# Performance work log

Measured on AMD Instinct MI355X. Metric: run time of the kernel, lower is better.

Reference implementation:

```python
import jax, jax.numpy as jnp
import numpy as np

B, H, W, C, N, P = 4, 200, 176, 256, 16384, 65536
EPS = 1e-3  # BatchNorm eps from the torch module


def _bn(x, g, b, axes):
    # training-mode batch norm (batch statistics), matching nn.BatchNorm forward
    m = x.mean(axes, keepdims=True)
    v = x.var(axes, keepdims=True)
    return (x - m) * jax.lax.rsqrt(v + EPS) * g + b


def setup_inputs() -> dict:
    key = jax.random.key(0)
    ks = jax.random.split(key, 16)
    s = 0.05
    d = {}
    d['feats'] = jax.random.normal(ks[0], (B, C, N), jnp.float32)
    d['cb'] = jax.random.randint(ks[1], (P,), 0, B, dtype=jnp.int32)
    d['cy'] = jax.random.randint(ks[2], (P,), 0, H, dtype=jnp.int32)
    d['cx'] = jax.random.randint(ks[3], (P,), 0, W, dtype=jnp.int32)
    # SH head: Linear(256,256,nb)+BN+ReLU, Linear(256,256,nb)+BN+ReLU, Linear(256,9,b)
    d['sh_w1'] = jax.random.normal(ks[4], (C, 256), jnp.float32) * s
    d['sh_g1'] = jnp.ones((256,), jnp.float32); d['sh_b1'] = jnp.zeros((256,), jnp.float32)
    d['sh_w2'] = jax.random.normal(ks[5], (256, 256), jnp.float32) * s
    d['sh_g2'] = jnp.ones((256,), jnp.float32); d['sh_b2'] = jnp.zeros((256,), jnp.float32)
    d['sh_w3'] = jax.random.normal(ks[6], (256, 9), jnp.float32) * s
    d['sh_bias3'] = jnp.zeros((9,), jnp.float32)
    # Gaus head: Linear(256,256,nb)+BN+ReLU, Linear(256,128,nb)+BN+ReLU, Linear(128,1,b)+sigmoid
    d['g_w1'] = jax.random.normal(ks[7], (C, 256), jnp.float32) * s
    d['g_g1'] = jnp.ones((256,), jnp.float32); d['g_b1'] = jnp.zeros((256,), jnp.float32)
    d['g_w2'] = jax.random.normal(ks[8], (256, 128), jnp.float32) * s
    d['g_g2'] = jnp.ones((128,), jnp.float32); d['g_b2'] = jnp.zeros((128,), jnp.float32)
    d['g_w3'] = jax.random.normal(ks[9], (128, 1), jnp.float32) * s
    d['g_bias3'] = jnp.zeros((1,), jnp.float32)
    # conv_out: 3x3 SparseConv2d no-bias + BN + ReLU ; shared_conv: 3x3 SubMConv2d bias + BN + ReLU
    d['cw1'] = jax.random.normal(ks[10], (3, 3, C, C), jnp.float32) * s
    d['c1_g'] = jnp.ones((C,), jnp.float32); d['c1_b'] = jnp.zeros((C,), jnp.float32)
    d['cw2'] = jax.random.normal(ks[11], (3, 3, C, C), jnp.float32) * s
    d['c2_bias'] = jnp.zeros((C,), jnp.float32)
    d['c2_g'] = jnp.ones((C,), jnp.float32); d['c2_b'] = jnp.zeros((C,), jnp.float32)
    return d


def reference(feats, cb, cy, cx, sh_w1, sh_g1, sh_b1, sh_w2, sh_g2, sh_b2, sh_w3, sh_bias3,
              g_w1, g_g1, g_b1, g_w2, g_g2, g_b2, g_w3, g_bias3,
              cw1, c1_g, c1_b, cw2, c2_bias, c2_g, c2_b):
    # [B,C,N] -> [B*N, C] point-wise features
    pw = feats.transpose(0, 2, 1).reshape(-1, C)
    # pool_feature_in_same_voxel: mean of point features sharing a voxel
    vid = cb * (H * W) + cy * W + cx  # [P] linear voxel id over dense BEV grid
    S = B * H * W
    sums = jax.ops.segment_sum(pw, vid, num_segments=S)            # [S, C]
    cnt = jax.ops.segment_sum(jnp.ones((P,), pw.dtype), vid, num_segments=S)
    pooled = sums / jnp.maximum(cnt, 1.0)[:, None]                 # [S, C]
    # SH head
    h = jax.nn.relu(_bn(pooled @ sh_w1, sh_g1, sh_b1, 0))
    h = jax.nn.relu(_bn(h @ sh_w2, sh_g2, sh_b2, 0))
    pred_sh = h @ sh_w3 + sh_bias3                                 # [S, 9]
    # Gaussian head
    g = jax.nn.relu(_bn(pooled @ g_w1, g_g1, g_b1, 0))
    g = jax.nn.relu(_bn(g @ g_w2, g_g2, g_b2, 0))
    pred_gaus = jax.nn.sigmoid(g @ g_w3 + g_bias3)                 # [S, 1]
    # get_sparse_voxel_feature3: SH (DC term) + gaussian modulated voxel features
    sp = pooled * pred_gaus * pred_sh[:, :1]                       # [S, C]
    x = sp.reshape(B, H, W, C)                                      # dense BEV sparse-tensor equivalent
    dn = ('NHWC', 'HWIO', 'NHWC')
    x = jax.lax.conv_general_dilated(x, cw1, (1, 1), 'SAME', dimension_numbers=dn)
    x = jax.nn.relu(_bn(x, c1_g, c1_b, (0, 1, 2)))
    x = jax.lax.conv_general_dilated(x, cw2, (1, 1), 'SAME', dimension_numbers=dn) + c2_bias
    x = jax.nn.relu(_bn(x, c2_g, c2_b, (0, 1, 2)))
    return x
```

## Files before the change

### kernel.cpp

```cpp
#include <hip/hip_runtime.h>
#include <hip/hip_bf16.h>
#include <cstdint>
#include <cstddef>

#define B_DIM 4
#define H_DIM 200
#define W_DIM 176
#define CCH 256
#define NPP 16384
#define NPTS 65536
#define HW 35200
#define S_TOT 140800
#define EPS 1e-3f
#define INV_S (1.0f/140800.0f)

typedef unsigned short ushort_t;
typedef __attribute__((ext_vector_type(8))) short bf16x8;
typedef __attribute__((ext_vector_type(4))) float f32x4;

__device__ __forceinline__ ushort_t f2bf(float f) {
    __hip_bfloat16 h = __float2bfloat16(f);
    return *(ushort_t*)&h;
}
__device__ __forceinline__ float bf2f(ushort_t u) {
    __hip_bfloat16 h = *(__hip_bfloat16*)&u;
    return __bfloat162float(h);
}

__device__ __forceinline__ void async16(const void* g, void* l) {
    __builtin_amdgcn_global_load_lds(
        (const __attribute__((address_space(1))) unsigned int*)g,
        (__attribute__((address_space(3))) unsigned int*)l,
        16, 0, 0);
}

__device__ __forceinline__ void wait_vmcnt0()  { asm volatile("s_waitcnt vmcnt(0)" ::: "memory"); }
__device__ __forceinline__ void wait_vmcnt4()  { asm volatile("s_waitcnt vmcnt(4)" ::: "memory"); }
__device__ __forceinline__ void wait_vmcnt8()  { asm volatile("s_waitcnt vmcnt(8)" ::: "memory"); }
__device__ __forceinline__ void wait_vmcnt10() { asm volatile("s_waitcnt vmcnt(10)" ::: "memory"); }
__device__ __forceinline__ void memfence_compiler() { asm volatile("" ::: "memory"); }

__device__ __forceinline__ int xcd_virt(int fid, int n) {
    int q = n >> 3, r = n & 7;
    int xcd = fid & 7, idx = fid >> 3;
    int base = (xcd < r) ? xcd * (q + 1) : r * (q + 1) + (xcd - r) * q;
    return base + idx;
}

__global__ __launch_bounds__(256) void k_transpose(
    const float* __restrict__ feats, ushort_t* __restrict__ FT)
{
    __shared__ float lds[64][65];
    const int b  = blockIdx.z;
    const int c0 = blockIdx.y * 64;
    const int n0 = blockIdx.x * 64;
    const int tid = threadIdx.x;
#pragma unroll
    for (int i = 0; i < 16; ++i) {
        int idx = i * 256 + tid;
        int cr = idx >> 6, nc = idx & 63;
        lds[cr][nc] = feats[((size_t)b * 256 + c0 + cr) * NPP + n0 + nc];
    }
    __syncthreads();
#pragma unroll
    for (int i = 0; i < 16; ++i) {
        int idx = i * 256 + tid;
        int nr = idx >> 6, cc = idx & 63;
        FT[((size_t)b * NPP + n0 + nr) * CCH + c0 + cc] = f2bf(lds[cc][nr]);
    }
}

__global__ __launch_bounds__(256) void k_buildidx(
    const int* __restrict__ cb, const int* __restrict__ cy,
    const int* __restrict__ cx, int* __restrict__ cnt,
    int* __restrict__ pslot, int* __restrict__ vid)
{
    int p = blockIdx.x * 256 + threadIdx.x;
    int v = cb[p] * HW + cy[p] * W_DIM + cx[p];
    vid[p] = v;
    int r = atomicAdd(&cnt[v], 1);
    if (r < 8) pslot[v * 8 + r] = p;
}

__global__ __launch_bounds__(256) void k_poolgather(
    const ushort_t* __restrict__ FT, const int* __restrict__ cnt,
    const int* __restrict__ pslot, const int* __restrict__ vid,
    ushort_t* __restrict__ Pb)
{
    const int wave = threadIdx.x >> 6;
    const int lane = threadIdx.x & 63;
    const int v = blockIdx.x * 4 + wave;
    const int c = cnt[v];
    float a0 = 0.f, a1 = 0.f, a2 = 0.f, a3 = 0.f;
    if (c <= 8) {
        for (int k = 0; k < c; ++k) {
            int p = pslot[v * 8 + k];
            ushort4 r = ((const ushort4*)(FT + (size_t)p * CCH))[lane];
            a0 += bf2f(r.x); a1 += bf2f(r.y); a2 += bf2f(r.z); a3 += bf2f(r.w);
        }
    } else {
        for (int p = 0; p < NPTS; ++p)
            if (vid[p] == v) {
                ushort4 r = ((const ushort4*)(FT + (size_t)p * CCH))[lane];
                a0 += bf2f(r.x); a1 += bf2f(r.y); a2 += bf2f(r.z); a3 += bf2f(r.w);
            }
    }
    float inv = c ? 1.f / (float)c : 0.f;
    ushort4 o;
    o.x = f2bf(a0 * inv); o.y = f2bf(a1 * inv);
    o.z = f2bf(a2 * inv); o.w = f2bf(a3 * inv);
    ((ushort4*)(Pb + (size_t)v * CCH))[lane] = o;
}

__global__ __launch_bounds__(256) void k_gemmma(
    const ushort_t* __restrict__ X, const ushort_t* __restrict__ Wt,
    ushort_t* __restrict__ Y1, ushort_t* __restrict__ Y2, int ldY,
    int bnh, int nblocks,
    float* __restrict__ acc0, float* __restrict__ acc1, int sqoff)
{
    __shared__ ushort_t Asm[2][128 * 64];
    __shared__ ushort_t Bsm[2][128 * 64];
    const int tid  = threadIdx.x;
    const int w    = tid >> 6;
    const int lane = tid & 63;
    const int virt = xcd_virt(blockIdx.x, nblocks);
    const int pi   = virt / bnh;
    const int bn   = (virt % bnh) * 128;
    const int bm   = pi * 128;
    const int wr   = (w >> 1) * 64;
    const int wc   = (w & 1) * 64;

    size_t aoff[4]; size_t boff[4];
#pragma unroll
    for (int j = 0; j < 4; ++j) {
        int row  = 32 * j + 8 * w + (lane >> 3);
        int qlog = (lane & 7) ^ (row & 7);
        aoff[j] = (size_t)(bm + row) * 256 + qlog * 8;
        boff[j] = (size_t)(bn + row) * 256 + qlog * 8;
    }
    const int lo = (w * 8) * 64;

#pragma unroll
    for (int j = 0; j < 4; ++j) async16(X + aoff[j], &Asm[0][(j * 32) * 64 + lo]);
#pragma unroll
    for (int j = 0; j < 4; ++j) async16(Wt + boff[j], &Bsm[0][(j * 32) * 64 + lo]);

    f32x4 acc[4][4] = {};
    for (int kc = 0; kc < 4; ++kc) {
        if (kc < 3) {
#pragma unroll
            for (int j = 0; j < 4; ++j)
                async16(X + aoff[j] + (kc + 1) * 64, &Asm[(kc + 1) & 1][(j * 32) * 64 + lo]);
#pragma unroll
            for (int j = 0; j < 4; ++j)
                async16(Wt + boff[j] + (kc + 1) * 64, &Bsm[(kc + 1) & 1][(j * 32) * 64 + lo]);
            wait_vmcnt8();
        } else {
            wait_vmcnt0();
        }
        __builtin_amdgcn_s_barrier();
        const ushort_t* Ac = Asm[kc & 1];
        const ushort_t* Bc = Bsm[kc & 1];
        __builtin_amdgcn_s_setprio(1);
#pragma unroll
        for (int ks = 0; ks < 2; ++ks) {
            const int q = ks * 4 + (lane >> 4);
            bf16x8 af[4], bfr[4];
#pragma unroll
            for (int i = 0; i < 4; ++i) {
                int ra = wr + i * 16 + (lane & 15);
                af[i] = *(const bf16x8*)&Ac[ra * 64 + ((q ^ (ra & 7)) * 8)];
            }
#pragma unroll
            for (int jn = 0; jn < 4; ++jn) {
                int rn = wc + jn * 16 + (lane & 15);
                bfr[jn] = *(const bf16x8*)&Bc[rn * 64 + ((q ^ (rn & 7)) * 8)];
            }
#pragma unroll
            for (int i = 0; i < 4; ++i)
#pragma unroll
                for (int jn = 0; jn < 4; ++jn)
                    acc[i][jn] = __builtin_amdgcn_mfma_f32_16x16x32_bf16(
                        af[i], bfr[jn], acc[i][jn], 0, 0, 0);
        }
        __builtin_amdgcn_s_setprio(0);
        memfence_compiler();
        __builtin_amdgcn_s_barrier();
    }
    __syncthreads();

    const int crow0 = bm + wr + (lane >> 4) * 4;
    const int ccol0 = bn + wc + (lane & 15);
    float ls[4] = {}, lq[4] = {};
#pragma unroll
    for (int i = 0; i < 4; ++i)
#pragma unroll
        for (int jn = 0; jn < 4; ++jn) {
            int col = ccol0 + jn * 16;
#pragma unroll
            for (int r = 0; r < 4; ++r) {
                float v = acc[i][jn][r];
                ls[jn] += v; lq[jn] += v * v;
                size_t row = (size_t)(crow0 + i * 16 + r);
                if (col < 256) Y1[row * ldY + col] = f2bf(v);
                else           Y2[row * ldY + col - 256] = f2bf(v);
            }
        }
#pragma unroll
    for (int jn = 0; jn < 4; ++jn) {
        ls[jn] += __shfl_xor(ls[jn], 16, 64); ls[jn] += __shfl_xor(ls[jn], 32, 64);
        lq[jn] += __shfl_xor(lq[jn], 16, 64); lq[jn] += __shfl_xor(lq[jn], 32, 64);
    }
    float* red = (float*)&Asm[0][0];
    if (lane < 16) {
#pragma unroll
        for (int jn = 0; jn < 4; ++jn) {
            red[((w * 16 + lane) * 4 + jn) * 2 + 0] = ls[jn];
            red[((w * 16 + lane) * 4 + jn) * 2 + 1] = lq[jn];
        }
    }
    __syncthreads();
    if (tid < 256) {
        int colhalf = tid & 127, isq = tid >> 7;
        int pair = colhalf >> 6, within = colhalf & 63;
        int l16 = within & 15, jn = within >> 4;
        int w0 = pair ? 1 : 0, w1 = pair ? 3 : 2;
        float s = red[((w0 * 16 + l16) * 4 + jn) * 2 + isq]
                + red[((w1 * 16 + l16) * 4 + jn) * 2 + isq];
        int colg = bn + colhalf;
        float* t = (colg < 256) ? acc0 : acc1;
        atomicAdd(&t[(colg & 255) + isq * sqoff], s);
    }
}

__global__ __launch_bounds__(256) void k_convmma(
    const ushort_t* __restrict__ X, const ushort_t* __restrict__ Wt,
    ushort_t* __restrict__ Yb, const float* __restrict__ bias,
    const ushort_t* __restrict__ zp, float* __restrict__ accp)
{
    __shared__ ushort_t Asm[2][192 * 64];
    __shared__ ushort_t Bsm[2][128 * 64];
    const int tid  = threadIdx.x;
    const int w    = tid >> 6;
    const int lane = tid & 63;
    const int virt = xcd_virt(blockIdx.x, 2200);
    const int pi   = virt >> 1;
    const int bn   = (virt & 1) * 128;
    const int b    = pi / 275;
    const int rem  = pi % 275;
    const int th   = rem / 11, tw = rem % 11;
    const int y0   = th * 8 - 1, x0 = tw * 16 - 1;
    const int hb   = (w >> 1) * 4;
    const int wc   = (w & 1) * 64;

    const int qlog = (lane & 7) ^ (lane >> 3);
    const ushort_t* asrc[6];
#pragma unroll
    for (int j = 0; j < 6; ++j) {
        int hr = j * 32 + w * 8 + (lane >> 3);
        int ph = hr / 18, pw = hr % 18;
        int y = y0 + ph, x = x0 + pw;
        bool ok = (hr < 180) && ((unsigned)y < (unsigned)H_DIM) &&
                  ((unsigned)x < (unsigned)W_DIM);
        asrc[j] = ok ? X + ((size_t)b * HW + (size_t)y * W_DIM + x) * 256 + qlog * 8
                     : zp + (lane & 7) * 8;
    }
    const ushort_t* bsrc = Wt + (size_t)(bn + w * 8 + (lane >> 3)) * 256 + qlog * 8;
    const int lo = (w * 8) * 64;

#pragma unroll
    for (int j = 0; j < 6; ++j)
        async16(asrc[j], &Asm[0][(j * 32) * 64 + lo]);
#pragma unroll
    for (int j = 0; j < 4; ++j)
        async16(bsrc + (size_t)j * 8192, &Bsm[0][(j * 32) * 64 + lo]);

    f32x4 acc[4][4] = {};
    for (int kc = 0; kc < 4; ++kc) {
        const ushort_t* acur = Asm[kc & 1];
#pragma unroll
        for (int pos = 0; pos < 9; ++pos) {
            const ushort_t* bcur = Bsm[(kc + pos) & 1];
            ushort_t* bnxt = (ushort_t*)Bsm[(kc + pos + 1) & 1];
            if (pos == 0) {
                if (kc < 3) {
#pragma unroll
                    for (int j = 0; j < 6; ++j)
                        async16(asrc[j] + (kc + 1) * 64,
                                &Asm[(kc + 1) & 1][(j * 32) * 64 + lo]);
#pragma unroll
                    for (int j = 0; j < 4; ++j)
                        async16(bsrc + (size_t)65536 + kc * 64 + j * 8192,
                                bnxt + (j * 32) * 64 + lo);
                    wait_vmcnt10();
                } else {
#pragma unroll
                    for (int j = 0; j < 4; ++j)
                        async16(bsrc + (size_t)65536 + kc * 64 + j * 8192,
                                bnxt + (j * 32) * 64 + lo);
                    wait_vmcnt4();
                }
            } else if (pos < 8) {
#pragma unroll
                for (int j = 0; j < 4; ++j)
                    async16(bsrc + (size_t)(pos + 1) * 65536 + kc * 64 + j * 8192,
                            bnxt + (j * 32) * 64 + lo);
                wait_vmcnt4();
            } else if (kc < 3) {
#pragma unroll
                for (int j = 0; j < 4; ++j)
                    async16(bsrc + (size_t)(kc + 1) * 64 + j * 8192,
                            bnxt + (j * 32) * 64 + lo);
                wait_vmcnt4();
            } else {
                wait_vmcnt0();
            }
            __builtin_amdgcn_s_barrier();
            const int dy = pos / 3 - 1, dx = pos % 3 - 1;
            __builtin_amdgcn_s_setprio(1);
#pragma unroll
            for (int ks = 0; ks < 2; ++ks) {
                const int q = ks * 4 + (lane >> 4);
                bf16x8 af[4], bfr[4];
#pragma unroll
                for (int i = 0; i < 4; ++i) {
                    int ri = (hb + i + 1 + dy) * 18 + 1 + dx + (lane & 15);
                    af[i] = *(const bf16x8*)&acur[ri * 64 + ((q ^ (ri & 7)) * 8)];
                }
#pragma unroll
                for (int jn = 0; jn < 4; ++jn) {
                    int rn = wc + jn * 16 + (lane & 15);
                    bfr[jn] = *(const bf16x8*)&bcur[rn * 64 + ((q ^ (rn & 7)) * 8)];
                }
#pragma unroll
                for (int i = 0; i < 4; ++i)
#pragma unroll
                    for (int jn = 0; jn < 4; ++jn)
                        acc[i][jn] = __builtin_amdgcn_mfma_f32_16x16x32_bf16(
                            af[i], bfr[jn], acc[i][jn], 0, 0, 0);
            }
            __builtin_amdgcn_s_setprio(0);
            memfence_compiler();
            __builtin_amdgcn_s_barrier();
        }
    }
    __syncthreads();

    const size_t sbase = (size_t)b * HW + (size_t)(th * 8) * W_DIM + tw * 16;
    const int colb = bn + wc + (lane & 15);
    const int wsub = (lane >> 4) * 4;
    float ls[4] = {}, lq[4] = {};
#pragma unroll
    for (int i = 0; i < 4; ++i) {
        int h = hb + i;
#pragma unroll
        for (int jn = 0; jn < 4; ++jn) {
            int col = colb + jn * 16;
            float bb = bias ? bias[col] : 0.f;
#pragma unroll
            for (int r = 0; r < 4; ++r) {
                size_t s = sbase + (size_t)h * W_DIM + wsub + r;
                float v = acc[i][jn][r] + bb;
                ls[jn] += v; lq[jn] += v * v;
                Yb[s * 256 + col] = f2bf(v);
            }
        }
    }
#pragma unroll
    for (int jn = 0; jn < 4; ++jn) {
        ls[jn] += __shfl_xor(ls[jn], 16, 64); ls[jn] += __shfl_xor(ls[jn], 32, 64);
        lq[jn] += __shfl_xor(lq[jn], 16, 64); lq[jn] += __shfl_xor(lq[jn], 32, 64);
    }
    float* red = (float*)&Asm[0][0];
    if (lane < 16) {
#pragma unroll
        for (int jn = 0; jn < 4; ++jn) {
            red[((w * 16 + lane) * 4 + jn) * 2 + 0] = ls[jn];
            red[((w * 16 + lane) * 4 + jn) * 2 + 1] = lq[jn];
        }
    }
    __syncthreads();
    if (tid < 256) {
        int colhalf = tid & 127, isq = tid >> 7;
        int pair = colhalf >> 6, within = colhalf & 63;
        int l16 = within & 15, jn = within >> 4;
        int w0 = pair ? 1 : 0, w1 = pair ? 3 : 2;
        float s = red[((w0 * 16 + l16) * 4 + jn) * 2 + isq]
                + red[((w1 * 16 + l16) * 4 + jn) * 2 + isq];
        atomicAdd(&accp[(bn + colhalf) + isq * 256], s);
    }
}

__global__ __launch_bounds__(256) void k_castw(
    const float* __restrict__ Wc, ushort_t* __restrict__ Wt, int CO)
{
    int pc = blockIdx.x;
    int co = pc % CO, pos = pc / CO, ci = threadIdx.x;
    Wt[(size_t)pc * 256 + ci] = f2bf(Wc[((size_t)pos * 256 + ci) * CO + co]);
}

__global__ void k_bnparams(const float* __restrict__ acc,
                           const float* __restrict__ g,
                           const float* __restrict__ b,
                           float* __restrict__ par, int ncols)
{
    int c = threadIdx.x;
    if (c >= ncols) return;
    float m = acc[c] * INV_S;
    float v = acc[ncols + c] * INV_S - m * m;
    float sc = g[c] * rsqrtf(v + EPS);
    par[c] = sc;
    par[ncols + c] = b[c] - m * sc;
}

__global__ __launch_bounds__(256) void k_bnrelu_bf(
    ushort_t* __restrict__ Y, const float* __restrict__ par)
{
    size_t q = (size_t)blockIdx.x * 256 + threadIdx.x;
    int c = (int)(q & 63) * 4;
    ushort4 u = ((ushort4*)Y)[q];
    u.x = f2bf(fmaxf(0.f, bf2f(u.x) * par[c + 0] + par[256 + c + 0]));
    u.y = f2bf(fmaxf(0.f, bf2f(u.y) * par[c + 1] + par[256 + c + 1]));
    u.z = f2bf(fmaxf(0.f, bf2f(u.z) * par[c + 2] + par[256 + c + 2]));
    u.w = f2bf(fmaxf(0.f, bf2f(u.w) * par[c + 3] + par[256 + c + 3]));
    ((ushort4*)Y)[q] = u;
}

__global__ __launch_bounds__(256) void k_headfin(
    const ushort_t* __restrict__ B2, const ushort_t* __restrict__ B3,
    const float* __restrict__ par1, const float* __restrict__ par3,
    const float* __restrict__ shw3, const float* __restrict__ shb3,
    const float* __restrict__ gw3, const float* __restrict__ gb3,
    const ushort_t* __restrict__ Pb, ushort_t* __restrict__ Xb)
{
    const int wave = threadIdx.x >> 6;
    const int lane = threadIdx.x & 63;
    const int s = blockIdx.x * 4 + wave;
    const ushort_t* b2 = B2 + (size_t)s * 256;
    const ushort_t* b3 = B3 + (size_t)s * 128;
    float d1 = 0.f, d2 = 0.f;
    {
        ushort4 u = ((const ushort4*)b2)[lane];
        int c = lane * 4;
        float v0 = fmaxf(0.f, bf2f(u.x) * par1[c + 0] + par1[256 + c + 0]);
        float v1 = fmaxf(0.f, bf2f(u.y) * par1[c + 1] + par1[256 + c + 1]);
        float v2 = fmaxf(0.f, bf2f(u.z) * par1[c + 2] + par1[256 + c + 2]);
        float v3 = fmaxf(0.f, bf2f(u.w) * par1[c + 3] + par1[256 + c + 3]);
        d1 = v0 * shw3[(c + 0) * 9] + v1 * shw3[(c + 1) * 9]
           + v2 * shw3[(c + 2) * 9] + v3 * shw3[(c + 3) * 9];
    }
    {
        ushort2 u = ((const ushort2*)b3)[lane];
        int c = lane * 2;
        float v0 = fmaxf(0.f, bf2f(u.x) * par3[c + 0] + par3[128 + c + 0]);
        float v1 = fmaxf(0.f, bf2f(u.y) * par3[c + 1] + par3[128 + c + 1]);
        d2 = v0 * gw3[c + 0] + v1 * gw3[c + 1];
    }
#pragma unroll
    for (int off = 32; off > 0; off >>= 1) {
        d1 += __shfl_down(d1, off, 64);
        d2 += __shfl_down(d2, off, 64);
    }
    d1 = __shfl(d1, 0, 64);
    d2 = __shfl(d2, 0, 64);
    float shdc = d1 + shb3[0];
    float gaus = 1.f / (1.f + expf(-(d2 + gb3[0])));
    float factor = shdc * gaus;
    ushort4 pv = ((const ushort4*)(Pb + (size_t)s * 256))[lane];
    ushort4 o;
    o.x = f2bf(bf2f(pv.x) * factor);
    o.y = f2bf(bf2f(pv.y) * factor);
    o.z = f2bf(bf2f(pv.z) * factor);
    o.w = f2bf(bf2f(pv.w) * factor);
    ((ushort4*)(Xb + (size_t)s * 256))[lane] = o;
}

__global__ __launch_bounds__(256) void k_bnrelu_f32out(
    const ushort_t* __restrict__ Y, const float* __restrict__ par,
    float* __restrict__ out)
{
    size_t q = (size_t)blockIdx.x * 256 + threadIdx.x;
    int c = (int)(q & 63) * 4;
    ushort4 u = ((const ushort4*)Y)[q];
    float4 v;
    v.x = fmaxf(0.f, bf2f(u.x) * par[c + 0] + par[256 + c + 0]);
    v.y = fmaxf(0.f, bf2f(u.y) * par[c + 1] + par[256 + c + 1]);
    v.z = fmaxf(0.f, bf2f(u.z) * par[c + 2] + par[256 + c + 2]);
    v.w = fmaxf(0.f, bf2f(u.w) * par[c + 3] + par[256 + c + 3]);
    ((float4*)out)[q] = v;
}

extern "C" void kernel_launch(void* const* d_in, const int* in_sizes, int n_in,
                              void* d_out, int out_size, void* d_ws, size_t ws_size,
                              hipStream_t stream)
{
    (void)in_sizes; (void)n_in; (void)out_size; (void)ws_size;
    const float* feats   = (const float*)d_in[0];
    const int*   cb      = (const int*)d_in[1];
    const int*   cy      = (const int*)d_in[2];
    const int*   cx      = (const int*)d_in[3];
    const float* sh_w1   = (const float*)d_in[4];
    const float* sh_g1   = (const float*)d_in[5];
    const float* sh_b1   = (const float*)d_in[6];
    const float* sh_w2   = (const float*)d_in[7];
    const float* sh_g2   = (const float*)d_in[8];
    const float* sh_b2   = (const float*)d_in[9];
    const float* sh_w3   = (const float*)d_in[10];
    const float* sh_bias3= (const float*)d_in[11];
    const float* g_w1    = (const float*)d_in[12];
    const float* g_g1    = (const float*)d_in[13];
    const float* g_b1    = (const float*)d_in[14];
    const float* g_w2    = (const float*)d_in[15];
    const float* g_g2    = (const float*)d_in[16];
    const float* g_b2    = (const float*)d_in[17];
    const float* g_w3    = (const float*)d_in[18];
    const float* g_bias3 = (const float*)d_in[19];
    const float* cw1     = (const float*)d_in[20];
    const float* c1_g    = (const float*)d_in[21];
    const float* c1_b    = (const float*)d_in[22];
    const float* cw2     = (const float*)d_in[23];
    const float* c2_bias = (const float*)d_in[24];
    const float* c2_g    = (const float*)d_in[25];
    const float* c2_b    = (const float*)d_in[26];

    float* out = (float*)d_out;
    float* ws  = (float*)d_ws;
    ushort_t* Pb   = (ushort_t*)(ws);
    ushort_t* Bsh  = (ushort_t*)(ws + 18022400);
    ushort_t* Bg   = (ushort_t*)(ws + 36044800);
    ushort_t* Cb   = (ushort_t*)(ws + 54067200);
    ushort_t* FT   = (ushort_t*)(ws + 54067200);
    ushort_t* Db   = (ushort_t*)(ws + 72089600);
    int*      CNTi = (int*)(ws + 72089600);
    int*      PSL  = CNTi + S_TOT;
    int*      VID  = PSL + S_TOT * 8;
    ushort_t* Eb   = Pb;
    ushort_t* WCAT = (ushort_t*)(ws + 81100800);
    ushort_t* WS2  = WCAT + 131072;
    ushort_t* WG2  = WS2 + 65536;
    ushort_t* WT1  = WG2 + 32768;
    ushort_t* WT2  = WT1 + 589824;
    ushort_t* ZP   = WT2 + 589824;
    float*    ACC  = (float*)(ZP + 2048);
    float*    PAR  = ACC + 6 * 512;

    hipMemsetAsync(CNTi, 0, (size_t)S_TOT * 4, stream);
    hipMemsetAsync(ACC, 0, 6 * 512 * 4, stream);
    hipMemsetAsync(ZP, 0, 4096, stream);

    k_castw<<<256, 256, 0, stream>>>(sh_w1, WCAT, 256);
    k_castw<<<256, 256, 0, stream>>>(g_w1, WCAT + 65536, 256);
    k_castw<<<256, 256, 0, stream>>>(sh_w2, WS2, 256);
    k_castw<<<128, 256, 0, stream>>>(g_w2, WG2, 128);
    k_castw<<<9 * 256, 256, 0, stream>>>(cw1, WT1, 256);
    k_castw<<<9 * 256, 256, 0, stream>>>(cw2, WT2, 256);

    k_transpose<<<dim3(256, 4, 4), 256, 0, stream>>>(feats, FT);
    k_buildidx<<<NPTS / 256, 256, 0, stream>>>(cb, cy, cx, CNTi, PSL, VID);
    k_poolgather<<<S_TOT / 4, 256, 0, stream>>>(FT, CNTi, PSL, VID, Pb);

    k_gemmma<<<4400, 256, 0, stream>>>(Pb, WCAT, Bsh, Bg, 256, 4, 4400,
                                       ACC + 0 * 512, ACC + 2 * 512, 256);
    k_bnparams<<<1, 256, 0, stream>>>(ACC + 0 * 512, sh_g1, sh_b1, PAR + 0 * 512, 256);
    k_bnparams<<<1, 256, 0, stream>>>(ACC + 2 * 512, g_g1, g_b1, PAR + 2 * 512, 256);
    k_bnrelu_bf<<<35200, 256, 0, stream>>>(Bsh, PAR + 0 * 512);
    k_bnrelu_bf<<<35200, 256, 0, stream>>>(Bg, PAR + 2 * 512);
    k_gemmma<<<2200, 256, 0, stream>>>(Bsh, WS2, Cb, Cb, 256, 2, 2200,
                                       ACC + 1 * 512, ACC + 1 * 512, 256);
    k_bnparams<<<1, 256, 0, stream>>>(ACC + 1 * 512, sh_g2, sh_b2, PAR + 1 * 512, 256);
    k_gemmma<<<1100, 256, 0, stream>>>(Bg, WG2, Db, Db, 128, 1, 1100,
                                       ACC + 3 * 512, ACC + 3 * 512, 128);
    k_bnparams<<<1, 128, 0, stream>>>(ACC + 3 * 512, g_g2, g_b2, PAR + 3 * 512, 128);
    k_headfin<<<S_TOT / 4, 256, 0, stream>>>(Cb, Db, PAR + 1 * 512, PAR + 3 * 512,
                                             sh_w3, sh_bias3, g_w3, g_bias3, Pb, Bsh);
    k_convmma<<<2200, 256, 0, stream>>>(Bsh, WT1, Eb, nullptr, ZP, ACC + 4 * 512);
    k_bnparams<<<1, 256, 0, stream>>>(ACC + 4 * 512, c1_g, c1_b, PAR + 4 * 512, 256);
    k_bnrelu_bf<<<35200, 256, 0, stream>>>(Eb, PAR + 4 * 512);
    k_convmma<<<2200, 256, 0, stream>>>(Eb, WT2, Bsh, c2_bias, ZP, ACC + 5 * 512);
    k_bnparams<<<1, 256, 0, stream>>>(ACC + 5 * 512, c2_g, c2_b, PAR + 5 * 512, 256);
    k_bnrelu_f32out<<<35200, 256, 0, stream>>>(Bsh, PAR + 5 * 512, out);
}
```

Baseline: 811.6 us.

## Fuse BatchNorm+ReLU into consumer GEMM/conv loads and fold BN param kernels

```diff
diff --git a/kernel.cpp b/kernel.cpp
--- a/kernel.cpp
+++ b/kernel.cpp
@@ -38,7 +38,19 @@
 __device__ __forceinline__ void wait_vmcnt4()  { asm volatile("s_waitcnt vmcnt(4)" ::: "memory"); }
 __device__ __forceinline__ void wait_vmcnt8()  { asm volatile("s_waitcnt vmcnt(8)" ::: "memory"); }
 __device__ __forceinline__ void wait_vmcnt10() { asm volatile("s_waitcnt vmcnt(10)" ::: "memory"); }
+__device__ __forceinline__ void wait_lgkm0()   { asm volatile("s_waitcnt lgkmcnt(0)" ::: "memory"); }
 __device__ __forceinline__ void memfence_compiler() { asm volatile("" ::: "memory"); }
+
+__device__ __forceinline__ bf16x8 bnrelu8(bf16x8 a, const float* __restrict__ sc,
+                                          const float* __restrict__ sh) {
+    bf16x8 r;
+#pragma unroll
+    for (int e = 0; e < 8; ++e) {
+        float f = bf2f((ushort_t)a[e]);
+        r[e] = (short)f2bf(fmaxf(0.f, f * sc[e] + sh[e]));
+    }
+    return r;
+}
 
 __device__ __forceinline__ int xcd_virt(int fid, int n) {
     int q = n >> 3, r = n & 7;
@@ -230,6 +242,154 @@
         int colg = bn + colhalf;
         float* t = (colg < 256) ? acc0 : acc1;
         atomicAdd(&t[(colg & 255) + isq * sqoff], s);
+    }
+}
+
+__global__ __launch_bounds__(256) void k_gemmma_bn(
+    const ushort_t* __restrict__ X, const float* __restrict__ accIn,
+    const float* __restrict__ gIn, const float* __restrict__ bIn,
+    const ushort_t* __restrict__ Wt,
+    ushort_t* __restrict__ Y, int ldY, int bnh, int nblocks,
+    float* __restrict__ accOut, int sqoff)
+{
+    __shared__ ushort_t Asm[2][128 * 64];
+    __shared__ ushort_t Bsm[2][128 * 64];
+    __shared__ float parS[512];
+    const int tid  = threadIdx.x;
+    const int w    = tid >> 6;
+    const int lane = tid & 63;
+    {
+        float m = accIn[tid] * INV_S;
+        float v = accIn[256 + tid] * INV_S - m * m;
+        float sc = gIn[tid] * rsqrtf(v + EPS);
+        parS[tid] = sc;
+        parS[256 + tid] = bIn[tid] - m * sc;
+    }
+    __syncthreads();
+
+    const int virt = xcd_virt(blockIdx.x, nblocks);
+    const int pi   = virt / bnh;
+    const int bn   = (virt % bnh) * 128;
+    const int bm   = pi * 128;
+    const int wr   = (w >> 1) * 64;
+    const int wc   = (w & 1) * 64;
+
+    const int qlog = (lane & 7) ^ ((8 * w + (lane >> 3)) & 7);
+    size_t aoff[4]; size_t boff[4]; int arow[4];
+#pragma unroll
+    for (int j = 0; j < 4; ++j) {
+        int row  = 32 * j + 8 * w + (lane >> 3);
+        arow[j] = row;
+        aoff[j] = (size_t)(bm + row) * 256 + qlog * 8;
+        boff[j] = (size_t)(bn + row) * 256 + qlog * 8;
+    }
+    const int lo = (w * 8) * 64;
+    const int lsub = (lane & 7) * 8;
+
+    bf16x8 ar[2][4];
+#pragma unroll
+    for (int j = 0; j < 4; ++j) async16(Wt + boff[j], &Bsm[0][(j * 32) * 64 + lo]);
+#pragma unroll
+    for (int j = 0; j < 4; ++j) ar[0][j] = *(const bf16x8*)(X + aoff[j]);
+    {
+        const int cb = qlog * 8;
+#pragma unroll
+        for (int j = 0; j < 4; ++j)
+            *(bf16x8*)&Asm[0][arow[j] * 64 + lsub] =
+                bnrelu8(ar[0][j], parS + cb, parS + 256 + cb);
+    }
+    wait_lgkm0();
+
+    f32x4 acc[4][4] = {};
+#pragma unroll
+    for (int kc = 0; kc < 4; ++kc) {
+        if (kc < 3) {
+#pragma unroll
+            for (int j = 0; j < 4; ++j)
+                async16(Wt + boff[j] + (kc + 1) * 64, &Bsm[(kc + 1) & 1][(j * 32) * 64 + lo]);
+#pragma unroll
+            for (int j = 0; j < 4; ++j)
+                ar[(kc + 1) & 1][j] = *(const bf16x8*)(X + aoff[j] + (kc + 1) * 64);
+            wait_vmcnt8();
+        } else {
+            wait_vmcnt0();
+        }
+        __builtin_amdgcn_s_barrier();
+        const ushort_t* Ac = Asm[kc & 1];
+        const ushort_t* Bc = Bsm[kc & 1];
+        __builtin_amdgcn_s_setprio(1);
+#pragma unroll
+        for (int ks = 0; ks < 2; ++ks) {
+            const int q = ks * 4 + (lane >> 4);
+            bf16x8 af[4], bfr[4];
+#pragma unroll
+            for (int i = 0; i < 4; ++i) {
+                int ra = wr + i * 16 + (lane & 15);
+                af[i] = *(const bf16x8*)&Ac[ra * 64 + ((q ^ (ra & 7)) * 8)];
+            }
+#pragma unroll
+            for (int jn = 0; jn < 4; ++jn) {
+                int rn = wc + jn * 16 + (lane & 15);
+                bfr[jn] = *(const bf16x8*)&Bc[rn * 64 + ((q ^ (rn & 7)) * 8)];
+            }
+#pragma unroll
+            for (int i = 0; i < 4; ++i)
+#pragma unroll
+                for (int jn = 0; jn < 4; ++jn)
+                    acc[i][jn] = __builtin_amdgcn_mfma_f32_16x16x32_bf16(
+                        af[i], bfr[jn], acc[i][jn], 0, 0, 0);
+        }
+        __builtin_amdgcn_s_setprio(0);
+        if (kc < 3) {
+            const int cb = (kc + 1) * 64 + qlog * 8;
+#pragma unroll
+            for (int j = 0; j < 4; ++j)
+                *(bf16x8*)&Asm[(kc + 1) & 1][arow[j] * 64 + lsub] =
+                    bnrelu8(ar[(kc + 1) & 1][j], parS + cb, parS + 256 + cb);
+            wait_lgkm0();
+        }
+        memfence_compiler();
+        __builtin_amdgcn_s_barrier();
+    }
+    __syncthreads();
+
+    const int crow0 = bm + wr + (lane >> 4) * 4;
+    const int ccol0 = bn + wc + (lane & 15);
+    float ls[4] = {}, lq[4] = {};
+#pragma unroll
+    for (int i = 0; i < 4; ++i)
+#pragma unroll
+        for (int jn = 0; jn < 4; ++jn) {
+            int col = ccol0 + jn * 16;
+#pragma unroll
+            for (int r = 0; r < 4; ++r) {
+                float v = acc[i][jn][r];
+                ls[jn] += v; lq[jn] += v * v;
+                Y[(size_t)(crow0 + i * 16 + r) * ldY + col] = f2bf(v);
+            }
+        }
+#pragma unroll
+    for (int jn = 0; jn < 4; ++jn) {
+        ls[jn] += __shfl_xor(ls[jn], 16, 64); ls[jn] += __shfl_xor(ls[jn], 32, 64);
+        lq[jn] += __shfl_xor(lq[jn], 16, 64); lq[jn] += __shfl_xor(lq[jn], 32, 64);
+    }
+    float* red = (float*)&Asm[0][0];
+    if (lane < 16) {
+#pragma unroll
+        for (int jn = 0; jn < 4; ++jn) {
+            red[((w * 16 + lane) * 4 + jn) * 2 + 0] = ls[jn];
+            red[((w * 16 + lane) * 4 + jn) * 2 + 1] = lq[jn];
+        }
+    }
+    __syncthreads();
+    if (tid < 256) {
+        int colhalf = tid & 127, isq = tid >> 7;
+        int pair = colhalf >> 6, within = colhalf & 63;
+        int l16 = within & 15, jn = within >> 4;
+        int w0 = pair ? 1 : 0, w1 = pair ? 3 : 2;
+        float s = red[((w0 * 16 + l16) * 4 + jn) * 2 + isq]
+                + red[((w1 * 16 + l16) * 4 + jn) * 2 + isq];
+        atomicAdd(&accOut[(bn + colhalf) + isq * sqoff], s);
     }
 }
 
@@ -391,6 +551,173 @@
     }
 }
 
+__global__ __launch_bounds__(256) void k_convmma_bn(
+    const ushort_t* __restrict__ X, const float* __restrict__ par,
+    const ushort_t* __restrict__ Wt,
+    ushort_t* __restrict__ Yb, const float* __restrict__ bias,
+    const ushort_t* __restrict__ zp, float* __restrict__ accp)
+{
+    __shared__ ushort_t Asm[2][192 * 64];
+    __shared__ ushort_t Bsm[2][128 * 64];
+    const int tid  = threadIdx.x;
+    const int w    = tid >> 6;
+    const int lane = tid & 63;
+    const int virt = xcd_virt(blockIdx.x, 2200);
+    const int pi   = virt >> 1;
+    const int bn   = (virt & 1) * 128;
+    const int b    = pi / 275;
+    const int rem  = pi % 275;
+    const int th   = rem / 11, tw = rem % 11;
+    const int y0   = th * 8 - 1, x0 = tw * 16 - 1;
+    const int hb   = (w >> 1) * 4;
+    const int wc   = (w & 1) * 64;
+
+    const int qlog = (lane & 7) ^ (lane >> 3);
+    const ushort_t* asrc[6];
+    bool okj[6];
+    int arow[6];
+#pragma unroll
+    for (int j = 0; j < 6; ++j) {
+        int hr = j * 32 + w * 8 + (lane >> 3);
+        arow[j] = hr;
+        int ph = hr / 18, pw = hr % 18;
+        int y = y0 + ph, x = x0 + pw;
+        okj[j] = (hr < 180) && ((unsigned)y < (unsigned)H_DIM) &&
+                 ((unsigned)x < (unsigned)W_DIM);
+        asrc[j] = okj[j] ? X + ((size_t)b * HW + (size_t)y * W_DIM + x) * 256 + qlog * 8
+                         : zp + (lane & 7) * 8;
+    }
+    const ushort_t* bsrc = Wt + (size_t)(bn + w * 8 + (lane >> 3)) * 256 + qlog * 8;
+    const int lo = (w * 8) * 64;
+    const int lsub = (lane & 7) * 8;
+    const bf16x8 zv = 0;
+
+    bf16x8 areg[6];
+#pragma unroll
+    for (int j = 0; j < 6; ++j) areg[j] = *(const bf16x8*)(asrc[j]);
+#pragma unroll
+    for (int j = 0; j < 4; ++j)
+        async16(bsrc + (size_t)j * 8192, &Bsm[0][(j * 32) * 64 + lo]);
+    {
+        const int cb = qlog * 8;
+#pragma unroll
+        for (int j = 0; j < 6; ++j)
+            *(bf16x8*)&Asm[0][arow[j] * 64 + lsub] =
+                okj[j] ? bnrelu8(areg[j], par + cb, par + 256 + cb) : zv;
+    }
+    wait_lgkm0();
+
+    f32x4 acc[4][4] = {};
+#pragma unroll
+    for (int kc = 0; kc < 4; ++kc) {
+        const ushort_t* acur = Asm[kc & 1];
+#pragma unroll
+        for (int pos = 0; pos < 9; ++pos) {
+            const ushort_t* bcur = Bsm[(kc + pos) & 1];
+            ushort_t* bnxt = (ushort_t*)Bsm[(kc + pos + 1) & 1];
+            if (pos < 8) {
+#pragma unroll
+                for (int j = 0; j < 4; ++j)
+                    async16(bsrc + (size_t)(pos + 1) * 65536 + kc * 64 + j * 8192,
+                            bnxt + (j * 32) * 64 + lo);
+            } else if (kc < 3) {
+#pragma unroll
+                for (int j = 0; j < 4; ++j)
+                    async16(bsrc + (size_t)(kc + 1) * 64 + j * 8192,
+                            bnxt + (j * 32) * 64 + lo);
+            }
+            if (pos == 5 && kc < 3) {
+#pragma unroll
+                for (int j = 0; j < 6; ++j)
+                    areg[j] = *(const bf16x8*)(asrc[j] + (kc + 1) * 64);
+            }
+            if (kc == 3 && pos == 8)      wait_vmcnt0();
+            else if (pos == 6 && kc < 3)  wait_vmcnt10();
+            else                          wait_vmcnt4();
+            __builtin_amdgcn_s_barrier();
+            const int dy = pos / 3 - 1, dx = pos % 3 - 1;
+            __builtin_amdgcn_s_setprio(1);
+#pragma unroll
+            for (int ks = 0; ks < 2; ++ks) {
+                const int q = ks * 4 + (lane >> 4);
+                bf16x8 af[4], bfr[4];
+#pragma unroll
+                for (int i = 0; i < 4; ++i) {
+                    int ri = (hb + i + 1 + dy) * 18 + 1 + dx + (lane & 15);
+                    af[i] = *(const bf16x8*)&acur[ri * 64 + ((q ^ (ri & 7)) * 8)];
+                }
+#pragma unroll
+                for (int jn = 0; jn < 4; ++jn) {
+                    int rn = wc + jn * 16 + (lane & 15);
+                    bfr[jn] = *(const bf16x8*)&bcur[rn * 64 + ((q ^ (rn & 7)) * 8)];
+                }
+#pragma unroll
+                for (int i = 0; i < 4; ++i)
+#pragma unroll
+                    for (int jn = 0; jn < 4; ++jn)
+                        acc[i][jn] = __builtin_amdgcn_mfma_f32_16x16x32_bf16(
+                            af[i], bfr[jn], acc[i][jn], 0, 0, 0);
+            }
+            __builtin_amdgcn_s_setprio(0);
+            if (pos == 8 && kc < 3) {
+                const int cb = (kc + 1) * 64 + qlog * 8;
+#pragma unroll
+                for (int j = 0; j < 6; ++j)
+                    *(bf16x8*)&Asm[(kc + 1) & 1][arow[j] * 64 + lsub] =
+                        okj[j] ? bnrelu8(areg[j], par + cb, par + 256 + cb) : zv;
+                wait_lgkm0();
+            }
+            memfence_compiler();
+            __builtin_amdgcn_s_barrier();
+        }
+    }
+    __syncthreads();
+
+    const size_t sbase = (size_t)b * HW + (size_t)(th * 8) * W_DIM + tw * 16;
+    const int colb = bn + wc + (lane & 15);
+    const int wsub = (lane >> 4) * 4;
+    float ls[4] = {}, lq[4] = {};
+#pragma unroll
+    for (int i = 0; i < 4; ++i) {
+        int h = hb + i;
+#pragma unroll
+        for (int jn = 0; jn < 4; ++jn) {
+            int col = colb + jn * 16;
+            float bb = bias ? bias[col] : 0.f;
+#pragma unroll
+            for (int r = 0; r < 4; ++r) {
+                size_t s = sbase + (size_t)h * W_DIM + wsub + r;
+                float v = acc[i][jn][r] + bb;
+                ls[jn] += v; lq[jn] += v * v;
+                Yb[s * 256 + col] = f2bf(v);
+            }
+        }
+    }
+#pragma unroll
+    for (int jn = 0; jn < 4; ++jn) {
+        ls[jn] += __shfl_xor(ls[jn], 16, 64); ls[jn] += __shfl_xor(ls[jn], 32, 64);
+        lq[jn] += __shfl_xor(lq[jn], 16, 64); lq[jn] += __shfl_xor(lq[jn], 32, 64);
+    }
+    float* red = (float*)&Asm[0][0];
+    if (lane < 16) {
+#pragma unroll
+        for (int jn = 0; jn < 4; ++jn) {
+            red[((w * 16 + lane) * 4 + jn) * 2 + 0] = ls[jn];
+            red[((w * 16 + lane) * 4 + jn) * 2 + 1] = lq[jn];
+        }
+    }
+    __syncthreads();
+    if (tid < 256) {
+        int colhalf = tid & 127, isq = tid >> 7;
+        int pair = colhalf >> 6, within = colhalf & 63;
+        int l16 = within & 15, jn = within >> 4;
+        int w0 = pair ? 1 : 0, w1 = pair ? 3 : 2;
+        float s = red[((w0 * 16 + l16) * 4 + jn) * 2 + isq]
+                + red[((w1 * 16 + l16) * 4 + jn) * 2 + isq];
+        atomicAdd(&accp[(bn + colhalf) + isq * 256], s);
+    }
+}
+
 __global__ __launch_bounds__(256) void k_castw(
     const float* __restrict__ Wc, ushort_t* __restrict__ Wt, int CO)
 {
@@ -413,28 +740,34 @@
     par[ncols + c] = b[c] - m * sc;
 }
 
-__global__ __launch_bounds__(256) void k_bnrelu_bf(
-    ushort_t* __restrict__ Y, const float* __restrict__ par)
-{
-    size_t q = (size_t)blockIdx.x * 256 + threadIdx.x;
-    int c = (int)(q & 63) * 4;
-    ushort4 u = ((ushort4*)Y)[q];
-    u.x = f2bf(fmaxf(0.f, bf2f(u.x) * par[c + 0] + par[256 + c + 0]));
-    u.y = f2bf(fmaxf(0.f, bf2f(u.y) * par[c + 1] + par[256 + c + 1]));
-    u.z = f2bf(fmaxf(0.f, bf2f(u.z) * par[c + 2] + par[256 + c + 2]));
-    u.w = f2bf(fmaxf(0.f, bf2f(u.w) * par[c + 3] + par[256 + c + 3]));
-    ((ushort4*)Y)[q] = u;
-}
-
 __global__ __launch_bounds__(256) void k_headfin(
     const ushort_t* __restrict__ B2, const ushort_t* __restrict__ B3,
-    const float* __restrict__ par1, const float* __restrict__ par3,
+    const float* __restrict__ acc1, const float* __restrict__ shg2,
+    const float* __restrict__ shb2,
+    const float* __restrict__ acc3, const float* __restrict__ gg2,
+    const float* __restrict__ gb2,
     const float* __restrict__ shw3, const float* __restrict__ shb3,
     const float* __restrict__ gw3, const float* __restrict__ gb3,
     const ushort_t* __restrict__ Pb, ushort_t* __restrict__ Xb)
 {
-    const int wave = threadIdx.x >> 6;
-    const int lane = threadIdx.x & 63;
+    __shared__ float parA[512], parB[256];
+    const int t = threadIdx.x;
+    {
+        float m = acc1[t] * INV_S;
+        float v = acc1[256 + t] * INV_S - m * m;
+        float sc = shg2[t] * rsqrtf(v + EPS);
+        parA[t] = sc; parA[256 + t] = shb2[t] - m * sc;
+    }
+    if (t < 128) {
+        float m = acc3[t] * INV_S;
+        float v = acc3[128 + t] * INV_S - m * m;
+        float sc = gg2[t] * rsqrtf(v + EPS);
+        parB[t] = sc; parB[128 + t] = gb2[t] - m * sc;
+    }
+    __syncthreads();
+
+    const int wave = t >> 6;
+    const int lane = t & 63;
     const int s = blockIdx.x * 4 + wave;
     const ushort_t* b2 = B2 + (size_t)s * 256;
     const ushort_t* b3 = B3 + (size_t)s * 128;
@@ -442,18 +775,18 @@
     {
         ushort4 u = ((const ushort4*)b2)[lane];
         int c = lane * 4;
-        float v0 = fmaxf(0.f, bf2f(u.x) * par1[c + 0] + par1[256 + c + 0]);
-        float v1 = fmaxf(0.f, bf2f(u.y) * par1[c + 1] + par1[256 + c + 1]);
-        float v2 = fmaxf(0.f, bf2f(u.z) * par1[c + 2] + par1[256 + c + 2]);
-        float v3 = fmaxf(0.f, bf2f(u.w) * par1[c + 3] + par1[256 + c + 3]);
+        float v0 = fmaxf(0.f, bf2f(u.x) * parA[c + 0] + parA[256 + c + 0]);
+        float v1 = fmaxf(0.f, bf2f(u.y) * parA[c + 1] + parA[256 + c + 1]);
+        float v2 = fmaxf(0.f, bf2f(u.z) * parA[c + 2] + parA[256 + c + 2]);
+        float v3 = fmaxf(0.f, bf2f(u.w) * parA[c + 3] + parA[256 + c + 3]);
         d1 = v0 * shw3[(c + 0) * 9] + v1 * shw3[(c + 1) * 9]
            + v2 * shw3[(c + 2) * 9] + v3 * shw3[(c + 3) * 9];
     }
     {
         ushort2 u = ((const ushort2*)b3)[lane];
         int c = lane * 2;
-        float v0 = fmaxf(0.f, bf2f(u.x) * par3[c + 0] + par3[128 + c + 0]);
-        float v1 = fmaxf(0.f, bf2f(u.y) * par3[c + 1] + par3[128 + c + 1]);
+        float v0 = fmaxf(0.f, bf2f(u.x) * parB[c + 0] + parB[128 + c + 0]);
+        float v1 = fmaxf(0.f, bf2f(u.y) * parB[c + 1] + parB[128 + c + 1]);
         d2 = v0 * gw3[c + 0] + v1 * gw3[c + 1];
     }
 #pragma unroll
@@ -476,10 +809,20 @@
 }
 
 __global__ __launch_bounds__(256) void k_bnrelu_f32out(
-    const ushort_t* __restrict__ Y, const float* __restrict__ par,
+    const ushort_t* __restrict__ Y, const float* __restrict__ acc5,
+    const float* __restrict__ g, const float* __restrict__ b,
     float* __restrict__ out)
 {
-    size_t q = (size_t)blockIdx.x * 256 + threadIdx.x;
+    __shared__ float par[512];
+    const int t = threadIdx.x;
+    {
+        float m = acc5[t] * INV_S;
+        float v = acc5[256 + t] * INV_S - m * m;
+        float sc = g[t] * rsqrtf(v + EPS);
+        par[t] = sc; par[256 + t] = b[t] - m * sc;
+    }
+    __syncthreads();
+    size_t q = (size_t)blockIdx.x * 256 + t;
     int c = (int)(q & 63) * 4;
     ushort4 u = ((const ushort4*)Y)[q];
     float4 v;
@@ -561,22 +904,20 @@
 
     k_gemmma<<<4400, 256, 0, stream>>>(Pb, WCAT, Bsh, Bg, 256, 4, 4400,
                                        ACC + 0 * 512, ACC + 2 * 512, 256);
-    k_bnparams<<<1, 256, 0, stream>>>(ACC + 0 * 512, sh_g1, sh_b1, PAR + 0 * 512, 256);
-    k_bnparams<<<1, 256, 0, stream>>>(ACC + 2 * 512, g_g1, g_b1, PAR + 2 * 512, 256);
-    k_bnrelu_bf<<<35200, 256, 0, stream>>>(Bsh, PAR + 0 * 512);
-    k_bnrelu_bf<<<35200, 256, 0, stream>>>(Bg, PAR + 2 * 512);
-    k_gemmma<<<2200, 256, 0, stream>>>(Bsh, WS2, Cb, Cb, 256, 2, 2200,
-                                       ACC + 1 * 512, ACC + 1 * 512, 256);
-    k_bnparams<<<1, 256, 0, stream>>>(ACC + 1 * 512, sh_g2, sh_b2, PAR + 1 * 512, 256);
-    k_gemmma<<<1100, 256, 0, stream>>>(Bg, WG2, Db, Db, 128, 1, 1100,
-                                       ACC + 3 * 512, ACC + 3 * 512, 128);
-    k_bnparams<<<1, 128, 0, stream>>>(ACC + 3 * 512, g_g2, g_b2, PAR + 3 * 512, 128);
-    k_headfin<<<S_TOT / 4, 256, 0, stream>>>(Cb, Db, PAR + 1 * 512, PAR + 3 * 512,
-                                             sh_w3, sh_bias3, g_w3, g_bias3, Pb, Bsh);
+    k_gemmma_bn<<<2200, 256, 0, stream>>>(Bsh, ACC + 0 * 512, sh_g1, sh_b1,
+                                          WS2, Cb, 256, 2, 2200,
+                                          ACC + 1 * 512, 256);
+    k_gemmma_bn<<<1100, 256, 0, stream>>>(Bg, ACC + 2 * 512, g_g1, g_b1,
+                                          WG2, Db, 128, 1, 1100,
+                                          ACC + 3 * 512, 128);
+    k_headfin<<<S_TOT / 4, 256, 0, stream>>>(Cb, Db,
+                                             ACC + 1 * 512, sh_g2, sh_b2,
+                                             ACC + 3 * 512, g_g2, g_b2,
+                                             sh_w3, sh_bias3, g_w3, g_bias3,
+                                             Pb, Bsh);
     k_convmma<<<2200, 256, 0, stream>>>(Bsh, WT1, Eb, nullptr, ZP, ACC + 4 * 512);
-    k_bnparams<<<1, 256, 0, stream>>>(ACC + 4 * 512, c1_g, c1_b, PAR + 4 * 512, 256);
-    k_bnrelu_bf<<<35200, 256, 0, stream>>>(Eb, PAR + 4 * 512);
-    k_convmma<<<2200, 256, 0, stream>>>(Eb, WT2, Bsh, c2_bias, ZP, ACC + 5 * 512);
-    k_bnparams<<<1, 256, 0, stream>>>(ACC + 5 * 512, c2_g, c2_b, PAR + 5 * 512, 256);
-    k_bnrelu_f32out<<<35200, 256, 0, stream>>>(Bsh, PAR + 5 * 512, out);
-}
+    k_bnparams<<<1, 256, 0, stream>>>(ACC + 4 * 512, c1_g, c1_b, PAR, 256);
+    k_convmma_bn<<<2200, 256, 0, stream>>>(Eb, PAR, WT2, Bsh, c2_bias, ZP,
+                                           ACC + 5 * 512);
+    k_bnrelu_f32out<<<35200, 256, 0, stream>>>(Bsh, ACC + 5 * 512, c2_g, c2_b, out);
+}
```

Result: faster. 750.7 us (-7.5%).
